# Performance work log

Hardware: AMD Instinct MI355X
Metric: run time of the kernel (lower is better)

## Reference

```python
import jax, jax.numpy as jnp
import numpy as np

N = 10000
E = 320000
C = 16


def gcn_conv(x, edge_index, W, b, num_nodes):
    # PyG GCNConv: h = X W, then symmetric-normalized aggregation with self-loops, then + b
    h = x @ W  # [N, F_out]
    loop = jnp.arange(num_nodes, dtype=edge_index.dtype)
    src = jnp.concatenate([edge_index[0], loop])
    dst = jnp.concatenate([edge_index[1], loop])
    ones = jnp.ones(src.shape[0], dtype=h.dtype)
    deg = jax.ops.segment_sum(ones, dst, num_segments=num_nodes)  # in-degree incl. self-loop
    dinv = jnp.where(deg > 0, jax.lax.rsqrt(deg), 0.0)
    norm = dinv[src] * dinv[dst]  # [E+N]
    msg = h[src] * norm[:, None]  # gather + scale
    out = jax.ops.segment_sum(msg, dst, num_segments=num_nodes)  # scatter-add
    return out + b


def setup_inputs() -> dict:
    key = jax.random.key(0)
    ks = jax.random.split(key, 8)
    x = jax.random.normal(ks[0], (N, N), dtype=jnp.float32)
    edge_index = jax.random.randint(ks[1], (2, E), 0, N, dtype=jnp.int64)
    W1 = jax.random.normal(ks[2], (N, 64), dtype=jnp.float32) * (1.0 / np.sqrt(N))
    b1 = jnp.zeros((64,), dtype=jnp.float32)
    W2 = jax.random.normal(ks[3], (64, 64), dtype=jnp.float32) * (1.0 / 8.0)
    b2 = jnp.zeros((64,), dtype=jnp.float32)
    W3 = jax.random.normal(ks[4], (64, C), dtype=jnp.float32) * (1.0 / 8.0)
    b3 = jnp.zeros((C,), dtype=jnp.float32)
    return {"x": x, "edge_index": edge_index, "W1": W1, "b1": b1,
            "W2": W2, "b2": b2, "W3": W3, "b3": b3}


def reference(x, edge_index, W1, b1, W2, b2, W3, b3):
    h = jax.nn.relu(gcn_conv(x, edge_index, W1, b1, N))
    h = jax.nn.relu(gcn_conv(h, edge_index, W2, b2, N))
    h = gcn_conv(h, edge_index, W3, b3, N)
    return jax.nn.softmax(h, axis=1)
```

## Files before the change

### kernel.cpp

```cpp
#include <hip/hip_runtime.h>

#define N_NODES 10000
#define E_EDGES 320000
#define KP 10016

typedef float f32x4 __attribute__((ext_vector_type(4)));
typedef __bf16 bf16x8 __attribute__((ext_vector_type(8)));

union frag_u { int4 i; bf16x8 b; };

static __device__ __forceinline__ ushort f2bf(float f) {
    unsigned u = __float_as_uint(f);
    unsigned r = (u + 0x7fffu + ((u >> 16) & 1u)) >> 16;
    return (ushort)r;
}
static __device__ __forceinline__ float bf2f(ushort h) {
    return __uint_as_float(((unsigned)h) << 16);
}

static __device__ __forceinline__ void split2(float f0, float f1,
                                              unsigned& hi, unsigned& lo) {
    unsigned u0 = __float_as_uint(f0), u1 = __float_as_uint(f1);
    hi = __builtin_amdgcn_perm(u1, u0, 0x07060302u);
    float h0 = __uint_as_float(u0 & 0xFFFF0000u);
    float h1 = __uint_as_float(u1 & 0xFFFF0000u);
    float l0 = f0 - h0, l1 = f1 - h1;
    lo = __builtin_amdgcn_perm(__float_as_uint(l1), __float_as_uint(l0), 0x07060302u);
}

static __device__ __forceinline__ void load16_to_lds(const float* gp, void* lp) {
    __builtin_amdgcn_global_load_lds(
        (__attribute__((address_space(1))) void*)(gp),
        (__attribute__((address_space(3))) void*)(lp), 16, 0, 0);
}


#define HIST_BLOCKS (E_EDGES / 256)
#define WSPLIT_KB   ((KP + 255) / 256)
#define WSPLIT_BLOCKS (WSPLIT_KB * 64)

__global__ void k_hist_wsplit(const int* __restrict__ dst, int* __restrict__ deg,
                              const float* __restrict__ W1, ushort* __restrict__ Whi,
                              ushort* __restrict__ Wlo) {
    int bid = blockIdx.x;
    int tid = threadIdx.x;
    if (bid < HIST_BLOCKS) {
        int e = bid * 256 + tid;
        atomicAdd(&deg[dst[e]], 1);
    } else {
        int q = bid - HIST_BLOCKS;
        int n = q / WSPLIT_KB;
        int kb = q % WSPLIT_KB;
        int k = kb * 256 + tid;
        if (k >= KP) return;
        ushort h = 0, l = 0;
        if (k < N_NODES) {
            float f = W1[(long)k * 64 + n];
            h = f2bf(f);
            l = f2bf(f - bf2f(h));
        }
        Whi[(long)n * KP + k] = h;
        Wlo[(long)n * KP + k] = l;
    }
}


__global__ void k_scan(const int* __restrict__ deg, int* __restrict__ roff,
                       float* __restrict__ dinv) {
    __shared__ int sums[256];
    __shared__ int offs[256];
    const int CH = 40;
    int t = threadIdx.x;
    int base = t * CH;
    int s = 0;
    for (int i = 0; i < CH; i++) {
        int idx = base + i;
        if (idx < N_NODES) {
            int d = deg[idx];
            s += d;
            dinv[idx] = rsqrtf(1.0f + (float)d);
        }
    }
    sums[t] = s;
    __syncthreads();
    if (t == 0) {
        int r = 0;
        for (int i = 0; i < 256; i++) { offs[i] = r; r += sums[i]; }
    }
    __syncthreads();
    int r = offs[t];
    for (int i = 0; i < CH; i++) {
        int idx = base + i;
        if (idx < N_NODES) { roff[idx] = r; r += deg[idx]; }
    }
    if (t == 255) roff[N_NODES] = E_EDGES;
}

__global__ void k_scatter(const int* __restrict__ src, const int* __restrict__ dst,
                          const int* __restrict__ roff, int* __restrict__ cursor,
                          const float* __restrict__ dinv,
                          int* __restrict__ csrc, float* __restrict__ cw) {
    int e = blockIdx.x * blockDim.x + threadIdx.x;
    if (e >= E_EDGES) return;
    int s = src[e], d = dst[e];
    int slot = roff[d] + atomicAdd(&cursor[d], 1);
    csrc[slot] = s;
    cw[slot] = dinv[s] * dinv[d];
}


#define G1_BM 128
#define G1_CHUNK 640
#define G1_NCHUNK 16

__global__ __launch_bounds__(256) void k_gemm1_mfma(
        const float* __restrict__ x, const ushort* __restrict__ Whi,
        const ushort* __restrict__ Wlo, float* __restrict__ out) {
    __shared__ float As32[G1_BM][32];
    __shared__ ushort Bs[2][64][40];

    int tid = threadIdx.x;
    int lane = tid & 63, wv = tid >> 6;
    int quad = lane >> 4, lm = lane & 15;
    int m0 = blockIdx.x * G1_BM;
    int ks = blockIdx.y * G1_CHUNK;
    int ke = min(ks + G1_CHUNK, KP);

    int rown = lane >> 3;
    int sp = (lane & 7) ^ rown;
    long abase[4];
#pragma unroll
    for (int i = 0; i < 4; i++) {
        int row = (wv * 4 + i) * 8 + rown;
        int gm = min(m0 + row, N_NODES - 1);
        abase[i] = (long)gm * N_NODES + sp * 4;
    }
    const long FLAT_MAX = (long)N_NODES * N_NODES - 4;

    int bn = tid >> 2, bp = (tid & 3) * 8;
    const ushort* whip = Whi + (long)bn * KP + bp;
    const ushort* wlop = Wlo + (long)bn * KP + bp;

    f32x4 acc[2][4] = {};

    for (int k0 = ks; k0 < ke; k0 += 32) {
#pragma unroll
        for (int i = 0; i < 4; i++) {
            long flat = abase[i] + k0;
            if (flat > FLAT_MAX) flat = FLAT_MAX;
            load16_to_lds(x + flat, &As32[(wv * 4 + i) * 8][0]);
        }
        float4 vh = *(const float4*)(whip + k0);
        float4 vl = *(const float4*)(wlop + k0);
        *(float4*)&Bs[0][bn][bp] = vh;
        *(float4*)&Bs[1][bn][bp] = vl;
        __syncthreads();

        frag_u ah[2], al[2];
#pragma unroll
        for (int r = 0; r < 2; r++) {
            int row = wv * 32 + r * 16 + lm;
            int r7 = row & 7;
            int s0 = (quad * 2) ^ r7;
            int s1 = (quad * 2 + 1) ^ r7;
            float4 fa = *(const float4*)&As32[row][s0 * 4];
            float4 fb = *(const float4*)&As32[row][s1 * 4];
            unsigned h0, l0, h1, l1, h2, l2, h3, l3;
            split2(fa.x, fa.y, h0, l0);
            split2(fa.z, fa.w, h1, l1);
            split2(fb.x, fb.y, h2, l2);
            split2(fb.z, fb.w, h3, l3);
            ah[r].i = make_int4((int)h0, (int)h1, (int)h2, (int)h3);
            al[r].i = make_int4((int)l0, (int)l1, (int)l2, (int)l3);
        }
        frag_u bh[4], bl[4];
#pragma unroll
        for (int c = 0; c < 4; c++) {
            int n = c * 16 + lm;
            bh[c].b = *(const bf16x8*)&Bs[0][n][quad * 8];
            bl[c].b = *(const bf16x8*)&Bs[1][n][quad * 8];
        }
#pragma unroll
        for (int r = 0; r < 2; r++)
#pragma unroll
            for (int c = 0; c < 4; c++) {
                acc[r][c] = __builtin_amdgcn_mfma_f32_16x16x32_bf16(al[r].b, bh[c].b, acc[r][c], 0, 0, 0);
                acc[r][c] = __builtin_amdgcn_mfma_f32_16x16x32_bf16(ah[r].b, bl[c].b, acc[r][c], 0, 0, 0);
                acc[r][c] = __builtin_amdgcn_mfma_f32_16x16x32_bf16(ah[r].b, bh[c].b, acc[r][c], 0, 0, 0);
            }
        __syncthreads();
    }

#pragma unroll
    for (int r = 0; r < 2; r++)
#pragma unroll
        for (int c = 0; c < 4; c++) {
            int row0 = m0 + wv * 32 + r * 16 + quad * 4;
            int cn = c * 16 + lm;
#pragma unroll
            for (int i = 0; i < 4; i++) {
                int gm = row0 + i;
                if (gm < N_NODES) atomicAdd(&out[gm * 64 + cn], acc[r][c][i]);
            }
        }
}


__global__ void k_agg64(const float* __restrict__ h, const float* __restrict__ bias,
                        const int* __restrict__ roff, const int* __restrict__ csrc,
                        const float* __restrict__ cw, const float* __restrict__ dinv,
                        float* __restrict__ out, int do_relu) {
    int n = blockIdx.x * 4 + (threadIdx.x >> 6);
    int c = threadIdx.x & 63;
    float di = dinv[n];
    float acc = di * di * h[n * 64 + c];
    int e0 = roff[n], e1 = roff[n + 1];
    int e = e0;
    for (; e + 3 < e1; e += 4) {
        int s0 = csrc[e], s1 = csrc[e + 1], s2 = csrc[e + 2], s3 = csrc[e + 3];
        float w0 = cw[e], w1 = cw[e + 1], w2 = cw[e + 2], w3 = cw[e + 3];
        float v0 = h[s0 * 64 + c], v1 = h[s1 * 64 + c];
        float v2 = h[s2 * 64 + c], v3 = h[s3 * 64 + c];
        acc = fmaf(w0, v0, acc);
        acc = fmaf(w1, v1, acc);
        acc = fmaf(w2, v2, acc);
        acc = fmaf(w3, v3, acc);
    }
    for (; e < e1; e++)
        acc = fmaf(cw[e], h[csrc[e] * 64 + c], acc);
    acc += bias[c];
    if (do_relu) acc = fmaxf(acc, 0.f);
    out[n * 64 + c] = acc;
}


__global__ __launch_bounds__(256) void k_layer2(
        const float* __restrict__ h, const float* __restrict__ W2,
        const float* __restrict__ b2,
        const int* __restrict__ roff, const int* __restrict__ csrc,
        const float* __restrict__ cw, const float* __restrict__ dinv,
        float* __restrict__ out) {
    __shared__ float Ws[64 * 64];
    __shared__ float rowbuf[4][64];
    int tid = threadIdx.x;
    int w = tid >> 6, c = tid & 63;
    for (int f = tid; f < 1024; f += 256)
        *(float4*)&Ws[f * 4] = *(const float4*)&W2[f * 4];

    int n = blockIdx.x * 4 + w;
    float di = dinv[n];
    float acc = di * di * h[n * 64 + c];
    int e0 = roff[n], e1 = roff[n + 1];
    int e = e0;
    for (; e + 3 < e1; e += 4) {
        int s0 = csrc[e], s1 = csrc[e + 1], s2 = csrc[e + 2], s3 = csrc[e + 3];
        float w0 = cw[e], w1 = cw[e + 1], w2 = cw[e + 2], w3 = cw[e + 3];
        float v0 = h[s0 * 64 + c], v1 = h[s1 * 64 + c];
        float v2 = h[s2 * 64 + c], v3 = h[s3 * 64 + c];
        acc = fmaf(w0, v0, acc);
        acc = fmaf(w1, v1, acc);
        acc = fmaf(w2, v2, acc);
        acc = fmaf(w3, v3, acc);
    }
    for (; e < e1; e++)
        acc = fmaf(cw[e], h[csrc[e] * 64 + c], acc);
    rowbuf[w][c] = acc;
    __syncthreads();

    float o = b2[c];
#pragma unroll
    for (int k = 0; k < 64; k++)
        o = fmaf(rowbuf[w][k], Ws[k * 64 + c], o);
    o = fmaxf(o, 0.f);
    out[n * 64 + c] = o;
}


__global__ __launch_bounds__(256) void k_layer3(
        const float* __restrict__ h, const float* __restrict__ W3,
        const float* __restrict__ b3,
        const int* __restrict__ roff, const int* __restrict__ csrc,
        const float* __restrict__ cw, const float* __restrict__ dinv,
        float* __restrict__ out) {
    __shared__ float Ws[64 * 17];
    __shared__ float rowbuf[4][64];
    int tid = threadIdx.x;
    int w = tid >> 6, c = tid & 63;
    for (int f = tid; f < 1024; f += 256) {
        int kk = f >> 4, cc0 = f & 15;
        Ws[kk * 17 + cc0] = W3[f];
    }

    int n = blockIdx.x * 4 + w;
    float di = dinv[n];
    float acc = di * di * h[n * 64 + c];
    int e0 = roff[n], e1 = roff[n + 1];
    int e = e0;
    for (; e + 3 < e1; e += 4) {
        int s0 = csrc[e], s1 = csrc[e + 1], s2 = csrc[e + 2], s3 = csrc[e + 3];
        float w0 = cw[e], w1 = cw[e + 1], w2 = cw[e + 2], w3 = cw[e + 3];
        float v0 = h[s0 * 64 + c], v1 = h[s1 * 64 + c];
        float v2 = h[s2 * 64 + c], v3 = h[s3 * 64 + c];
        acc = fmaf(w0, v0, acc);
        acc = fmaf(w1, v1, acc);
        acc = fmaf(w2, v2, acc);
        acc = fmaf(w3, v3, acc);
    }
    for (; e < e1; e++)
        acc = fmaf(cw[e], h[csrc[e] * 64 + c], acc);
    rowbuf[w][c] = acc;
    __syncthreads();

    int cc = c & 15, g = c >> 4;
    float o = 0.f;
#pragma unroll
    for (int i = 0; i < 16; i++) {
        int k = g * 16 + i;
        o = fmaf(rowbuf[w][k], Ws[k * 17 + cc], o);
    }
    o += __shfl_xor(o, 16);
    o += __shfl_xor(o, 32);
    float logit = o + b3[cc];
    float m = logit;
    m = fmaxf(m, __shfl_xor(m, 1));
    m = fmaxf(m, __shfl_xor(m, 2));
    m = fmaxf(m, __shfl_xor(m, 4));
    m = fmaxf(m, __shfl_xor(m, 8));
    float ex = expf(logit - m);
    float s = ex;
    s += __shfl_xor(s, 1);
    s += __shfl_xor(s, 2);
    s += __shfl_xor(s, 4);
    s += __shfl_xor(s, 8);
    if (g == 0) out[n * 16 + cc] = ex / s;
}


extern "C" void kernel_launch(void* const* d_in, const int* in_sizes, int n_in,
                              void* d_out, int out_size, void* d_ws, size_t ws_size,
                              hipStream_t stream) {
    (void)in_sizes; (void)n_in; (void)out_size; (void)ws_size;
    const float* x  = (const float*)d_in[0];
    const int*   ei = (const int*)d_in[1];
    const float* W1 = (const float*)d_in[2];
    const float* b1 = (const float*)d_in[3];
    const float* W2 = (const float*)d_in[4];
    const float* b2 = (const float*)d_in[5];
    const float* W3 = (const float*)d_in[6];
    const float* b3 = (const float*)d_in[7];
    float* out = (float*)d_out;
    const int* esrc = ei;
    const int* edst = ei + E_EDGES;

    char* p = (char*)d_ws;
    size_t off = 0;
    auto alloc = [&](size_t b) -> void* {
        void* r = p + off;
        off += (b + 255) & ~(size_t)255;
        return r;
    };
    int*    deg    = (int*)alloc(N_NODES * 4);
    int*    cursor = (int*)alloc(N_NODES * 4);
    float*  bufA   = (float*)alloc(N_NODES * 64 * 4);
    int*    roff   = (int*)alloc((N_NODES + 1) * 4);
    float*  dinv   = (float*)alloc(N_NODES * 4);
    int*    csrc   = (int*)alloc(E_EDGES * 4);
    float*  cw     = (float*)alloc(E_EDGES * 4);
    float*  bufB   = (float*)alloc(N_NODES * 64 * 4);
    ushort* Whi    = (ushort*)alloc((size_t)64 * KP * 2);
    ushort* Wlo    = (ushort*)alloc((size_t)64 * KP * 2);

    size_t zlen = (size_t)((char*)(bufA + N_NODES * 64) - (char*)deg);
    hipMemsetAsync(deg, 0, zlen, stream);

    k_hist_wsplit<<<HIST_BLOCKS + WSPLIT_BLOCKS, 256, 0, stream>>>(edst, deg, W1, Whi, Wlo);
    k_scan<<<1, 256, 0, stream>>>(deg, roff, dinv);
    k_scatter<<<(E_EDGES + 255) / 256, 256, 0, stream>>>(esrc, edst, roff, cursor, dinv,
                                                         csrc, cw);

    k_gemm1_mfma<<<dim3((N_NODES + G1_BM - 1) / G1_BM, G1_NCHUNK), 256, 0, stream>>>(
        x, Whi, Wlo, bufA);
    k_agg64<<<N_NODES / 4, 256, 0, stream>>>(bufA, b1, roff, csrc, cw, dinv, bufB, 1);
    k_layer2<<<N_NODES / 4, 256, 0, stream>>>(bufB, W2, b2, roff, csrc, cw, dinv, bufA);
    k_layer3<<<N_NODES / 4, 256, 0, stream>>>(bufA, W3, b3, roff, csrc, cw, dinv, out);
}
```

Before: 687.0 us.

## Double-buffer gemm1 K loop and replace split-K atomics with partial-sum reduction

The first-layer MFMA GEMM now double-buffers its LDS tiles for A and B. The next K slice is fetched while the current one is multiplied, and the two full __syncthreads per iteration become one explicit waitcnt plus barrier. The split-K epilogue no longer does atomicAdd into one output. Each K chunk writes its own partial buffer, and a new k_reduce16 kernel sums the 16 partials. This trades contended atomics for a larger workspace, extra memory traffic and one more kernel launch, and it doubles LDS use per block, which may lower occupancy.

```diff
diff --git a/kernel.cpp b/kernel.cpp
--- a/kernel.cpp
+++ b/kernel.cpp
@@ -115,9 +115,9 @@
 
 __global__ __launch_bounds__(256) void k_gemm1_mfma(
         const float* __restrict__ x, const ushort* __restrict__ Whi,
-        const ushort* __restrict__ Wlo, float* __restrict__ out) {
-    __shared__ float As32[G1_BM][32];
-    __shared__ ushort Bs[2][64][40];
+        const ushort* __restrict__ Wlo, float* __restrict__ outP) {
+    __shared__ float As32[2][G1_BM][32];
+    __shared__ ushort Bs[2][2][64][40];
 
     int tid = threadIdx.x;
     int lane = tid & 63, wv = tid >> 6;
@@ -143,18 +143,35 @@
 
     f32x4 acc[2][4] = {};
 
+#pragma unroll
+    for (int i = 0; i < 4; i++) {
+        long flat = abase[i] + ks;
+        if (flat > FLAT_MAX) flat = FLAT_MAX;
+        load16_to_lds(x + flat, &As32[0][(wv * 4 + i) * 8][0]);
+    }
+    {
+        float4 vh = *(const float4*)(whip + ks);
+        float4 vl = *(const float4*)(wlop + ks);
+        *(float4*)&Bs[0][0][bn][bp] = vh;
+        *(float4*)&Bs[0][1][bn][bp] = vl;
+    }
+    __syncthreads();
+
+    int cur = 0;
     for (int k0 = ks; k0 < ke; k0 += 32) {
-#pragma unroll
-        for (int i = 0; i < 4; i++) {
-            long flat = abase[i] + k0;
-            if (flat > FLAT_MAX) flat = FLAT_MAX;
-            load16_to_lds(x + flat, &As32[(wv * 4 + i) * 8][0]);
-        }
-        float4 vh = *(const float4*)(whip + k0);
-        float4 vl = *(const float4*)(wlop + k0);
-        *(float4*)&Bs[0][bn][bp] = vh;
-        *(float4*)&Bs[1][bn][bp] = vl;
-        __syncthreads();
+        int kn = k0 + 32;
+        bool pf = (kn < ke);
+        float4 vh, vl;
+        if (pf) {
+#pragma unroll
+            for (int i = 0; i < 4; i++) {
+                long flat = abase[i] + kn;
+                if (flat > FLAT_MAX) flat = FLAT_MAX;
+                load16_to_lds(x + flat, &As32[cur ^ 1][(wv * 4 + i) * 8][0]);
+            }
+            vh = *(const float4*)(whip + kn);
+            vl = *(const float4*)(wlop + kn);
+        }
 
         frag_u ah[2], al[2];
 #pragma unroll
@@ -163,8 +180,8 @@
             int r7 = row & 7;
             int s0 = (quad * 2) ^ r7;
             int s1 = (quad * 2 + 1) ^ r7;
-            float4 fa = *(const float4*)&As32[row][s0 * 4];
-            float4 fb = *(const float4*)&As32[row][s1 * 4];
+            float4 fa = *(const float4*)&As32[cur][row][s0 * 4];
+            float4 fb = *(const float4*)&As32[cur][row][s1 * 4];
             unsigned h0, l0, h1, l1, h2, l2, h3, l3;
             split2(fa.x, fa.y, h0, l0);
             split2(fa.z, fa.w, h1, l1);
@@ -177,8 +194,8 @@
 #pragma unroll
         for (int c = 0; c < 4; c++) {
             int n = c * 16 + lm;
-            bh[c].b = *(const bf16x8*)&Bs[0][n][quad * 8];
-            bl[c].b = *(const bf16x8*)&Bs[1][n][quad * 8];
+            bh[c].b = *(const bf16x8*)&Bs[cur][0][n][quad * 8];
+            bl[c].b = *(const bf16x8*)&Bs[cur][1][n][quad * 8];
         }
 #pragma unroll
         for (int r = 0; r < 2; r++)
@@ -188,9 +205,18 @@
                 acc[r][c] = __builtin_amdgcn_mfma_f32_16x16x32_bf16(ah[r].b, bl[c].b, acc[r][c], 0, 0, 0);
                 acc[r][c] = __builtin_amdgcn_mfma_f32_16x16x32_bf16(ah[r].b, bh[c].b, acc[r][c], 0, 0, 0);
             }
-        __syncthreads();
-    }
-
+
+        if (pf) {
+            asm volatile("s_waitcnt vmcnt(0)" ::: "memory");
+            *(float4*)&Bs[cur ^ 1][0][bn][bp] = vh;
+            *(float4*)&Bs[cur ^ 1][1][bn][bp] = vl;
+        }
+        asm volatile("s_waitcnt vmcnt(0) lgkmcnt(0)" ::: "memory");
+        __builtin_amdgcn_s_barrier();
+        cur ^= 1;
+    }
+
+    float* op = outP + (long)blockIdx.y * ((long)N_NODES * 64);
 #pragma unroll
     for (int r = 0; r < 2; r++)
 #pragma unroll
@@ -200,9 +226,18 @@
 #pragma unroll
             for (int i = 0; i < 4; i++) {
                 int gm = row0 + i;
-                if (gm < N_NODES) atomicAdd(&out[gm * 64 + cn], acc[r][c][i]);
+                if (gm < N_NODES) op[(long)gm * 64 + cn] = acc[r][c][i];
             }
         }
+}
+
+__global__ void k_reduce16(const float* __restrict__ P, float* __restrict__ o) {
+    int i = blockIdx.x * 256 + threadIdx.x;
+    float s = 0.f;
+#pragma unroll
+    for (int j = 0; j < G1_NCHUNK; j++)
+        s += P[(long)j * (N_NODES * 64) + i];
+    o[i] = s;
 }
 
 
@@ -307,7 +342,7 @@
         acc = fmaf(w3, v3, acc);
     }
     for (; e < e1; e++)
-        acc = fmaf(cw[e], h[csrc[e] * 64 + c], acc);
+        acc = fmaf(cw[e], h[csrc[e] * 16 + c & 0 ? 0 : csrc[e] * 64 + c], acc);
     rowbuf[w][c] = acc;
     __syncthreads();
 
@@ -361,16 +396,17 @@
     };
     int*    deg    = (int*)alloc(N_NODES * 4);
     int*    cursor = (int*)alloc(N_NODES * 4);
-    float*  bufA   = (float*)alloc(N_NODES * 64 * 4);
     int*    roff   = (int*)alloc((N_NODES + 1) * 4);
     float*  dinv   = (float*)alloc(N_NODES * 4);
     int*    csrc   = (int*)alloc(E_EDGES * 4);
     float*  cw     = (float*)alloc(E_EDGES * 4);
-    float*  bufB   = (float*)alloc(N_NODES * 64 * 4);
+    float*  bufA   = (float*)alloc((size_t)N_NODES * 64 * 4);
+    float*  bufB   = (float*)alloc((size_t)N_NODES * 64 * 4);
     ushort* Whi    = (ushort*)alloc((size_t)64 * KP * 2);
     ushort* Wlo    = (ushort*)alloc((size_t)64 * KP * 2);
-
-    size_t zlen = (size_t)((char*)(bufA + N_NODES * 64) - (char*)deg);
+    float*  bufP   = (float*)alloc((size_t)G1_NCHUNK * N_NODES * 64 * 4);
+
+    size_t zlen = (size_t)((char*)(cursor + N_NODES) - (char*)deg);
     hipMemsetAsync(deg, 0, zlen, stream);
 
     k_hist_wsplit<<<HIST_BLOCKS + WSPLIT_BLOCKS, 256, 0, stream>>>(edst, deg, W1, Whi, Wlo);
@@ -379,7 +415,8 @@
                                                          csrc, cw);
 
     k_gemm1_mfma<<<dim3((N_NODES + G1_BM - 1) / G1_BM, G1_NCHUNK), 256, 0, stream>>>(
-        x, Whi, Wlo, bufA);
+        x, Whi, Wlo, bufP);
+    k_reduce16<<<(N_NODES * 64) / 256, 256, 0, stream>>>(bufP, bufA);
     k_agg64<<<N_NODES / 4, 256, 0, stream>>>(bufA, b1, roff, csrc, cw, dinv, bufB, 1);
     k_layer2<<<N_NODES / 4, 256, 0, stream>>>(bufB, W2, b2, roff, csrc, cw, dinv, bufA);
     k_layer3<<<N_NODES / 4, 256, 0, stream>>>(bufA, W3, b3, roff, csrc, cw, dinv, out);
```

Measured after the change: 695.9 us. Within noise of the previous version (+1.3%).
